# Performance work log

Measured on AMD Instinct MI355X. Metric: run time of the kernel, lower is better.

Reference implementation:

```python
import jax, jax.numpy as jnp
import numpy as np

N, E, D, H = 4096, 131072, 256, 8
DH = D // H  # head dim = 32


def layer_norm(x, g, b, eps=1e-5):
    mu = jnp.mean(x, axis=-1, keepdims=True)
    var = jnp.var(x, axis=-1, keepdims=True)
    return (x - mu) * jax.lax.rsqrt(var + eps) * g + b


def mlp2(x, w1, b1, w2, b2):
    # Linear -> GELU(exact) -> Linear (dropout is identity at inference)
    return jax.nn.gelu(x @ w1 + b1, approximate=False) @ w2 + b2


def setup_inputs() -> dict:
    key = jax.random.key(0)
    ks = iter(jax.random.split(key, 32))
    s = 0.02
    d = {
        'x': jax.random.normal(next(ks), (N, D), jnp.float32),
        'edge_index': jax.random.randint(next(ks), (2, E), 0, N, jnp.int32),
        'edge_attr': jax.random.normal(next(ks), (E, D), jnp.float32),
        # GINE eps
        'eps': jnp.zeros((1,), jnp.float32),
        # edge MLP (Linear weights stored [in, out])
        'e_w1': jax.random.normal(next(ks), (D, D), jnp.float32) * s,
        'e_b1': jnp.zeros((D,), jnp.float32),
        'e_w2': jax.random.normal(next(ks), (D, D), jnp.float32) * s,
        'e_b2': jnp.zeros((D,), jnp.float32),
        # update MLP
        'u_w1': jax.random.normal(next(ks), (D, D), jnp.float32) * s,
        'u_b1': jnp.zeros((D,), jnp.float32),
        'u_w2': jax.random.normal(next(ks), (D, D), jnp.float32) * s,
        'u_b2': jnp.zeros((D,), jnp.float32),
        # LayerNorms
        'ln_local_g': jnp.ones((D,), jnp.float32), 'ln_local_b': jnp.zeros((D,), jnp.float32),
        'ln_global_g': jnp.ones((D,), jnp.float32), 'ln_global_b': jnp.zeros((D,), jnp.float32),
        'ln_ffn_g': jnp.ones((D,), jnp.float32), 'ln_ffn_b': jnp.zeros((D,), jnp.float32),
        # MHA projections ([in, out])
        'wq': jax.random.normal(next(ks), (D, D), jnp.float32) * s,
        'wk': jax.random.normal(next(ks), (D, D), jnp.float32) * s,
        'wv': jax.random.normal(next(ks), (D, D), jnp.float32) * s,
        'bq': jnp.zeros((D,), jnp.float32), 'bk': jnp.zeros((D,), jnp.float32), 'bv': jnp.zeros((D,), jnp.float32),
        'wo': jax.random.normal(next(ks), (D, D), jnp.float32) * s,
        'bo': jnp.zeros((D,), jnp.float32),
        # FFN
        'f_w1': jax.random.normal(next(ks), (D, 4 * D), jnp.float32) * s,
        'f_b1': jnp.zeros((4 * D,), jnp.float32),
        'f_w2': jax.random.normal(next(ks), (4 * D, D), jnp.float32) * s,
        'f_b2': jnp.zeros((D,), jnp.float32),
    }
    return d


def reference(x, edge_index, edge_attr, eps,
              e_w1, e_b1, e_w2, e_b2, u_w1, u_b1, u_w2, u_b2,
              ln_local_g, ln_local_b, ln_global_g, ln_global_b, ln_ffn_g, ln_ffn_b,
              wq, wk, wv, bq, bk, bv, wo, bo,
              f_w1, f_b1, f_w2, f_b2):
    src, dst = edge_index[0], edge_index[1]
    n = x.shape[0]

    # ---- local GINE conv on pre-normed features ----
    h = layer_norm(x, ln_local_g, ln_local_b)
    messages = mlp2(h[src] + edge_attr, e_w1, e_b1, e_w2, e_b2)  # [E, D]
    aggregated = jax.ops.segment_sum(messages, dst, num_segments=n)  # [N, D]
    local = mlp2((1.0 + eps) * h + aggregated, u_w1, u_b1, u_w2, u_b2)
    x = x + local

    # ---- global multihead self-attention over all nodes ----
    g = layer_norm(x, ln_global_g, ln_global_b)
    q = (g @ wq + bq).reshape(n, H, DH)
    k = (g @ wk + bk).reshape(n, H, DH)
    v = (g @ wv + bv).reshape(n, H, DH)
    scores = jnp.einsum('nhd,mhd->hnm', q, k) / jnp.sqrt(jnp.float32(DH))
    attn = jax.nn.softmax(scores, axis=-1)
    ctx = jnp.einsum('hnm,mhd->nhd', attn, v).reshape(n, D)
    x = x + (ctx @ wo + bo)

    # ---- FFN ----
    x = x + mlp2(layer_norm(x, ln_ffn_g, ln_ffn_b), f_w1, f_b1, f_w2, f_b2)
    return x
```

## Files before the change

### kernel.cpp

```cpp
#include <hip/hip_runtime.h>
#include <math.h>

#define N_NODES 4096
#define N_EDGES 131072
#define XPAD    272

using bf16x8 = __attribute__((ext_vector_type(8))) __bf16;
using f32x4  = __attribute__((ext_vector_type(4))) float;
typedef unsigned short u16;

__device__ __forceinline__ u16 f2bf(float f) {
  union { __bf16 b; u16 u; } cv; cv.b = (__bf16)f; return cv.u;
}
__device__ __forceinline__ float bf2f(u16 h) {
  return __uint_as_float(((unsigned)h) << 16);
}
__device__ __forceinline__ float gelu_tanh(float x) {
  float t = x * x;
  float y = x * (1.5957691216057308f + 0.07135481627f * t);
  float e = __expf(y);
  return x - x / (1.0f + e);
}
__device__ __forceinline__ f32x4 mfma16(bf16x8 a, bf16x8 b, f32x4 c) {
  return __builtin_amdgcn_mfma_f32_16x16x32_bf16(a, b, c, 0, 0, 0);
}

struct WPtrs { const float* p[10]; };
struct OPtrs { float* o[4]; float* l; };

__global__ void setup_kernel(WPtrs w, u16* __restrict__ dst, float qscale,
                             const int* __restrict__ ei, int* __restrict__ deg,
                             const float* __restrict__ bq, const float* __restrict__ bk,
                             const float* __restrict__ bv, float* __restrict__ qkvbias) {
  int blk = blockIdx.x, t = threadIdx.x;
  if (blk < 512) {
    int tid = blk * 256 + t;
    int m, ci;
    if (tid < 32768)      { m = tid >> 13;                 ci = tid & 8191; }
    else if (tid < 57344) { m = 4 + ((tid - 32768) >> 13); ci = (tid - 32768) & 8191; }
    else if (tid < 65536) { m = 7; ci = tid - 57344; }
    else if (tid < 98304) { m = 8; ci = tid - 65536; }
    else                  { m = 9; ci = tid - 98304; }
    int Cols = (m == 8) ? 1024 : 256;
    int k8   = (m == 8) ? (ci >> 10) : (ci >> 8);
    int c    = (m == 8) ? (ci & 1023) : (ci & 255);
    const float* src = w.p[m] + (size_t)(k8 * 8) * Cols + c;
    float sc = (m == 4) ? qscale : 1.0f;
    u16 tmp[8];
#pragma unroll
    for (int j = 0; j < 8; ++j) tmp[j] = f2bf(src[(size_t)j * Cols] * sc);
    size_t off;
    if (m < 4)       off = (size_t)(m << 16) + (size_t)(k8 * 256 + c) * 8;
    else if (m < 7)  off = 262144 + (size_t)(k8 * 768 + (m - 4) * 256 + c) * 8;
    else if (m == 7) off = 458752 + (size_t)(k8 * 256 + c) * 8;
    else if (m == 8) off = 524288 + (size_t)(k8 * 1024 + c) * 8;
    else             off = 786432 + (size_t)(k8 * 256 + c) * 8;
    *(uint4*)(dst + off) = *(const uint4*)tmp;
  } else if (blk < 1024) {
    int e = (blk - 512) * 256 + t;
    atomicAdd(&deg[ei[N_EDGES + e]], 1);
  } else {
#pragma unroll
    for (int i = 0; i < 3; ++i) {
      int idx = i * 256 + t;
      qkvbias[idx] = idx < 256 ? bq[idx] * qscale : (idx < 512 ? bk[idx - 256] : bv[idx - 512]);
    }
  }
}

__global__ void scan_kernel(const int* __restrict__ deg, int* __restrict__ offs) {
  __shared__ int part[1024];
  int t = threadIdx.x;
  int base = t * 4;
  int a0 = deg[base], a1 = deg[base + 1], a2 = deg[base + 2], a3 = deg[base + 3];
  int s = a0 + a1 + a2 + a3;
  part[t] = s;
  __syncthreads();
  for (int off = 1; off < 1024; off <<= 1) {
    int v = (t >= off) ? part[t - off] : 0;
    __syncthreads();
    part[t] += v;
    __syncthreads();
  }
  int excl = part[t] - s;
  offs[base] = excl;
  offs[base + 1] = excl + a0;
  offs[base + 2] = excl + a0 + a1;
  offs[base + 3] = excl + a0 + a1 + a2;
  if (t == 1023) offs[4096] = part[1023];
}

__global__ void mid_kernel(const int* __restrict__ ei, const int* __restrict__ offs,
                           int* __restrict__ cnt, int* __restrict__ eperm,
                           int* __restrict__ dst_s, int* __restrict__ src_s,
                           const float* __restrict__ x, const float* __restrict__ g,
                           const float* __restrict__ b, float* __restrict__ hf,
                           u16* __restrict__ hb) {
  int blk = blockIdx.x, t = threadIdx.x;
  if (blk < 512) {
    int e = blk * 256 + t;
    int d = ei[N_EDGES + e];
    int p = offs[d] + atomicAdd(&cnt[d], 1);
    eperm[p] = e;
    dst_s[p] = d;
    src_s[p] = ei[e];
  } else {
    int row = blk - 512;
    float v = x[(size_t)row * 256 + t];
    float s1 = v, s2 = v * v;
#pragma unroll
    for (int o = 32; o > 0; o >>= 1) { s1 += __shfl_xor(s1, o); s2 += __shfl_xor(s2, o); }
    __shared__ float a1[4], a2[4];
    int wv = t >> 6, lane = t & 63;
    if (lane == 0) { a1[wv] = s1; a2[wv] = s2; }
    __syncthreads();
    s1 = a1[0] + a1[1] + a1[2] + a1[3];
    s2 = a2[0] + a2[1] + a2[2] + a2[3];
    float mean = s1 * (1.0f / 256.0f);
    float var  = s2 * (1.0f / 256.0f) - mean * mean;
    float rs = rsqrtf(var + 1e-5f);
    float o = (v - mean) * rs * g[t] + b[t];
    hf[(size_t)row * 256 + t] = o;
    hb[(size_t)row * 256 + t] = f2bf(o);
  }
}

__launch_bounds__(512, 4)
__global__ void edge_kernel(const u16* __restrict__ hb, const float* __restrict__ ea,
                            const int* __restrict__ eperm, const int* __restrict__ src_s,
                            const int* __restrict__ dst_s,
                            const u16* __restrict__ wp1, const float* __restrict__ b1,
                            const u16* __restrict__ wp2, const float* __restrict__ b2,
                            float* __restrict__ agg) {
  __shared__ __align__(16) u16 X[128 * XPAD];
  const f32x4 fzero = {0.f, 0.f, 0.f, 0.f};
  int t = threadIdx.x;
  int lane = t & 63, wv = t >> 6;
  int lr = lane & 15, lq = lane >> 4;
  int wr = wv >> 2, wc = wv & 3;
  int e0 = blockIdx.x * 128;
  int col0 = wc * 64;
  int row0 = wr * 64;

  const u16* b1ptr = wp1 + ((size_t)lq * 256 + col0 + lr) * 8;
  const u16* b2ptr = wp2 + ((size_t)lq * 256 + col0 + lr) * 8;
  bf16x8 bc[4], bn[4];
#pragma unroll
  for (int ct = 0; ct < 4; ++ct) bc[ct] = *(const bf16x8*)(b1ptr + ct * 128);

  int ci = (t & 31) * 8;
#pragma unroll
  for (int it = 0; it < 8; ++it) {
    int r = it * 16 + (t >> 5);
    int e = eperm[e0 + r];
    int s = src_s[e0 + r];
    const float* pa = ea + (size_t)e * 256 + ci;
    float4 a0 = *(const float4*)pa;
    float4 a1 = *(const float4*)(pa + 4);
    ushort4 h0 = *(const ushort4*)(hb + (size_t)s * 256 + ci);
    ushort4 h1 = *(const ushort4*)(hb + (size_t)s * 256 + ci + 4);
    u16 tmp[8];
    tmp[0] = f2bf(a0.x + bf2f(h0.x)); tmp[1] = f2bf(a0.y + bf2f(h0.y));
    tmp[2] = f2bf(a0.z + bf2f(h0.z)); tmp[3] = f2bf(a0.w + bf2f(h0.w));
    tmp[4] = f2bf(a1.x + bf2f(h1.x)); tmp[5] = f2bf(a1.y + bf2f(h1.y));
    tmp[6] = f2bf(a1.z + bf2f(h1.z)); tmp[7] = f2bf(a1.w + bf2f(h1.w));
    *(uint4*)&X[r * XPAD + ci] = *(const uint4*)tmp;
  }
  __syncthreads();

  f32x4 acc[4][4];
#pragma unroll
  for (int i = 0; i < 4; ++i)
#pragma unroll
    for (int j = 0; j < 4; ++j) acc[i][j] = fzero;

#pragma unroll
  for (int ks = 0; ks < 8; ++ks) {
    if (ks < 7) {
#pragma unroll
      for (int ct = 0; ct < 4; ++ct)
        bn[ct] = *(const bf16x8*)(b1ptr + (size_t)(ks + 1) * 8192 + ct * 128);
    }
    bf16x8 a[4];
#pragma unroll
    for (int rt = 0; rt < 4; ++rt)
      a[rt] = *(const bf16x8*)&X[(row0 + rt * 16 + lr) * XPAD + ks * 32 + lq * 8];
#pragma unroll
    for (int ct = 0; ct < 4; ++ct)
#pragma unroll
      for (int rt = 0; rt < 4; ++rt) acc[rt][ct] = mfma16(a[rt], bc[ct], acc[rt][ct]);
#pragma unroll
    for (int ct = 0; ct < 4; ++ct) bc[ct] = bn[ct];
  }
#pragma unroll
  for (int ct = 0; ct < 4; ++ct) bn[ct] = *(const bf16x8*)(b2ptr + ct * 128);
  __syncthreads();

#pragma unroll
  for (int ct = 0; ct < 4; ++ct) {
    int c = col0 + ct * 16 + lr;
    float bb = b1[c];
#pragma unroll
    for (int rt = 0; rt < 4; ++rt)
#pragma unroll
      for (int r = 0; r < 4; ++r) {
        int row = row0 + rt * 16 + lq * 4 + r;
        X[row * XPAD + c] = f2bf(gelu_tanh(acc[rt][ct][r] + bb));
      }
  }
#pragma unroll
  for (int ct = 0; ct < 4; ++ct) bc[ct] = bn[ct];
  __syncthreads();

#pragma unroll
  for (int i = 0; i < 4; ++i)
#pragma unroll
    for (int j = 0; j < 4; ++j) acc[i][j] = fzero;
#pragma unroll
  for (int ks = 0; ks < 8; ++ks) {
    if (ks < 7) {
#pragma unroll
      for (int ct = 0; ct < 4; ++ct)
        bn[ct] = *(const bf16x8*)(b2ptr + (size_t)(ks + 1) * 8192 + ct * 128);
    }
    bf16x8 a[4];
#pragma unroll
    for (int rt = 0; rt < 4; ++rt)
      a[rt] = *(const bf16x8*)&X[(row0 + rt * 16 + lr) * XPAD + ks * 32 + lq * 8];
#pragma unroll
    for (int ct = 0; ct < 4; ++ct)
#pragma unroll
      for (int rt = 0; rt < 4; ++rt) acc[rt][ct] = mfma16(a[rt], bc[ct], acc[rt][ct]);
#pragma unroll
    for (int ct = 0; ct < 4; ++ct) bc[ct] = bn[ct];
  }
  __syncthreads();

#pragma unroll
  for (int ct = 0; ct < 4; ++ct) {
    int c = col0 + ct * 16 + lr;
    float bb = b2[c];
#pragma unroll
    for (int rt = 0; rt < 4; ++rt)
#pragma unroll
      for (int r = 0; r < 4; ++r) {
        int row = row0 + rt * 16 + lq * 4 + r;
        X[row * XPAD + c] = f2bf(acc[rt][ct][r] + bb);
      }
  }
  __syncthreads();

  {
    int c4 = (t & 63) * 4;
    int rbeg = wv * 16;
    float run0 = 0.f, run1 = 0.f, run2 = 0.f, run3 = 0.f;
    int cur = dst_s[e0 + rbeg];
    for (int r = rbeg; r < rbeg + 16; ++r) {
      int d = dst_s[e0 + r];
      if (d != cur) {
        float* p = &agg[(size_t)cur * 256 + c4];
        atomicAdd(p + 0, run0); atomicAdd(p + 1, run1);
        atomicAdd(p + 2, run2); atomicAdd(p + 3, run3);
        run0 = run1 = run2 = run3 = 0.f;
        cur = d;
      }
      ushort4 xv = *(const ushort4*)&X[r * XPAD + c4];
      run0 += bf2f(xv.x); run1 += bf2f(xv.y); run2 += bf2f(xv.z); run3 += bf2f(xv.w);
    }
    float* p = &agg[(size_t)cur * 256 + c4];
    atomicAdd(p + 0, run0); atomicAdd(p + 1, run1);
    atomicAdd(p + 2, run2); atomicAdd(p + 3, run3);
  }
}

__launch_bounds__(256, 2)
__global__ void update_kernel(const float* __restrict__ hf, const float* __restrict__ agg,
                              const float* __restrict__ epsp, const float* __restrict__ xin,
                              const u16* __restrict__ wp1, const float* __restrict__ b1,
                              const u16* __restrict__ wp2, const float* __restrict__ b2,
                              const float* __restrict__ lng, const float* __restrict__ lnb,
                              float* __restrict__ x1, u16* __restrict__ gb) {
  __shared__ __align__(16) u16 X[64 * XPAD];
  __shared__ float S1[64][4], S2[64][4], MUs[64], RSs[64];
  const f32x4 fzero = {0.f, 0.f, 0.f, 0.f};
  int t = threadIdx.x;
  int lane = t & 63, wv = t >> 6;
  int lr = lane & 15, lq = lane >> 4;
  int n0 = blockIdx.x * 64;
  int col0 = wv * 64;
  float epv = 1.0f + epsp[0];
  const u16* b1ptr = wp1 + ((size_t)lq * 256 + col0 + lr) * 8;
  const u16* b2ptr = wp2 + ((size_t)lq * 256 + col0 + lr) * 8;
  bf16x8 bc[4], bn[4];
#pragma unroll
  for (int ct = 0; ct < 4; ++ct) bc[ct] = *(const bf16x8*)(b1ptr + ct * 128);
  {
    int c4 = (t & 63) * 4;
#pragma unroll
    for (int ii = 0; ii < 16; ++ii) {
      int r = ii * 4 + wv;
      float4 h = *(const float4*)(hf + (size_t)(n0 + r) * 256 + c4);
      float4 a = *(const float4*)(agg + (size_t)(n0 + r) * 256 + c4);
      *(ushort4*)&X[r * XPAD + c4] =
          make_ushort4(f2bf(epv * h.x + a.x), f2bf(epv * h.y + a.y),
                       f2bf(epv * h.z + a.z), f2bf(epv * h.w + a.w));
    }
  }
  __syncthreads();
  f32x4 acc[4][4];
#pragma unroll
  for (int i = 0; i < 4; ++i)
#pragma unroll
    for (int j = 0; j < 4; ++j) acc[i][j] = fzero;
#pragma unroll
  for (int ks = 0; ks < 8; ++ks) {
    if (ks < 7) {
#pragma unroll
      for (int ct = 0; ct < 4; ++ct)
        bn[ct] = *(const bf16x8*)(b1ptr + (size_t)(ks + 1) * 8192 + ct * 128);
    }
    bf16x8 a[4];
#pragma unroll
    for (int rt = 0; rt < 4; ++rt)
      a[rt] = *(const bf16x8*)&X[(rt * 16 + lr) * XPAD + ks * 32 + lq * 8];
#pragma unroll
    for (int ct = 0; ct < 4; ++ct)
#pragma unroll
      for (int rt = 0; rt < 4; ++rt) acc[rt][ct] = mfma16(a[rt], bc[ct], acc[rt][ct]);
#pragma unroll
    for (int ct = 0; ct < 4; ++ct) bc[ct] = bn[ct];
  }
#pragma unroll
  for (int ct = 0; ct < 4; ++ct) bn[ct] = *(const bf16x8*)(b2ptr + ct * 128);
  __syncthreads();
#pragma unroll
  for (int ct = 0; ct < 4; ++ct) {
    int c = col0 + ct * 16 + lr;
    float bb = b1[c];
#pragma unroll
    for (int rt = 0; rt < 4; ++rt)
#pragma unroll
      for (int r = 0; r < 4; ++r) {
        int row = rt * 16 + lq * 4 + r;
        X[row * XPAD + c] = f2bf(gelu_tanh(acc[rt][ct][r] + bb));
      }
  }
#pragma unroll
  for (int ct = 0; ct < 4; ++ct) bc[ct] = bn[ct];
  __syncthreads();
#pragma unroll
  for (int i = 0; i < 4; ++i)
#pragma unroll
    for (int j = 0; j < 4; ++j) acc[i][j] = fzero;
#pragma unroll
  for (int ks = 0; ks < 8; ++ks) {
    if (ks < 7) {
#pragma unroll
      for (int ct = 0; ct < 4; ++ct)
        bn[ct] = *(const bf16x8*)(b2ptr + (size_t)(ks + 1) * 8192 + ct * 128);
    }
    bf16x8 a[4];
#pragma unroll
    for (int rt = 0; rt < 4; ++rt)
      a[rt] = *(const bf16x8*)&X[(rt * 16 + lr) * XPAD + ks * 32 + lq * 8];
#pragma unroll
    for (int ct = 0; ct < 4; ++ct)
#pragma unroll
      for (int rt = 0; rt < 4; ++rt) acc[rt][ct] = mfma16(a[rt], bc[ct], acc[rt][ct]);
#pragma unroll
    for (int ct = 0; ct < 4; ++ct) bc[ct] = bn[ct];
  }
  float bb2[4];
#pragma unroll
  for (int ct = 0; ct < 4; ++ct) bb2[ct] = b2[col0 + ct * 16 + lr];
#pragma unroll
  for (int rt = 0; rt < 4; ++rt)
#pragma unroll
    for (int r = 0; r < 4; ++r) {
      int row = rt * 16 + lq * 4 + r;
      int grow = n0 + row;
      float p1 = 0.f, p2 = 0.f;
#pragma unroll
      for (int ct = 0; ct < 4; ++ct) {
        int c = col0 + ct * 16 + lr;
        float v = acc[rt][ct][r] + bb2[ct] + xin[(size_t)grow * 256 + c];
        x1[(size_t)grow * 256 + c] = v;
        acc[rt][ct][r] = v;
        p1 += v; p2 += v * v;
      }
#pragma unroll
      for (int o = 1; o < 16; o <<= 1) { p1 += __shfl_xor(p1, o); p2 += __shfl_xor(p2, o); }
      if (lr == 0) { S1[row][wv] = p1; S2[row][wv] = p2; }
    }
  __syncthreads();
  if (t < 64) {
    float s1 = S1[t][0] + S1[t][1] + S1[t][2] + S1[t][3];
    float s2 = S2[t][0] + S2[t][1] + S2[t][2] + S2[t][3];
    float mu = s1 * (1.0f / 256.0f);
    float var = s2 * (1.0f / 256.0f) - mu * mu;
    MUs[t] = mu;
    RSs[t] = rsqrtf(var + 1e-5f);
  }
  __syncthreads();
  float gv[4], bv[4];
#pragma unroll
  for (int ct = 0; ct < 4; ++ct) {
    int c = col0 + ct * 16 + lr;
    gv[ct] = lng[c]; bv[ct] = lnb[c];
  }
#pragma unroll
  for (int rt = 0; rt < 4; ++rt)
#pragma unroll
    for (int r = 0; r < 4; ++r) {
      int row = rt * 16 + lq * 4 + r;
      int grow = n0 + row;
      float mu = MUs[row], rs = RSs[row];
#pragma unroll
      for (int ct = 0; ct < 4; ++ct) {
        int c = col0 + ct * 16 + lr;
        gb[(size_t)grow * 256 + c] = f2bf((acc[rt][ct][r] - mu) * rs * gv[ct] + bv[ct]);
      }
    }
}

template <int ROWS, bool GELU_F, bool RES, bool OUTB, bool LNF, bool QKV>
__launch_bounds__(256, 2)
__global__ void gemm_kernel(const u16* __restrict__ A, int lda,
                            const u16* __restrict__ Wp, int K, int WCols,
                            const float* __restrict__ bias, float scale,
                            const float* __restrict__ res,
                            const float* __restrict__ lng, const float* __restrict__ lnb,
                            float* __restrict__ outf, u16* __restrict__ outh,
                            u16* __restrict__ outh2, u16* __restrict__ vtp, int ldo) {
  __shared__ __align__(16) u16 X[ROWS * XPAD];
  __shared__ float S1[LNF ? ROWS : 1][4], S2[LNF ? ROWS : 1][4];
  __shared__ float MUs[LNF ? ROWS : 1], RSs[LNF ? ROWS : 1];
  constexpr int RT = ROWS / 16;
  const f32x4 fzero = {0.f, 0.f, 0.f, 0.f};
  int t = threadIdx.x;
  int lane = t & 63, wv = t >> 6;
  int lr = lane & 15, lq = lane >> 4;
  int r0 = blockIdx.x * ROWS;
  int cb = blockIdx.y * 256;
  f32x4 acc[RT][4];
#pragma unroll
  for (int i = 0; i < RT; ++i)
#pragma unroll
    for (int j = 0; j < 4; ++j) acc[i][j] = fzero;
  const u16* bptr = Wp + ((size_t)lq * WCols + cb + wv * 64 + lr) * 8;
  bf16x8 bc[4], bn[4];
#pragma unroll
  for (int ct = 0; ct < 4; ++ct) bc[ct] = *(const bf16x8*)(bptr + ct * 128);
  int rr = t >> 5, c8 = (t & 31) * 8;
  for (int kc = 0; kc < K; kc += 256) {
#pragma unroll
    for (int ii = 0; ii < ROWS / 8; ++ii) {
      int r = ii * 8 + rr;
      *(uint4*)&X[r * XPAD + c8] = *(const uint4*)(A + (size_t)(r0 + r) * lda + kc + c8);
    }
    __syncthreads();
#pragma unroll
    for (int ks = 0; ks < 8; ++ks) {
      bool more = (ks < 7) || (kc + 256 < K);
      if (more) {
        size_t koff = (ks < 7) ? ((size_t)(kc >> 3) + (ks + 1) * 4) * WCols
                               : ((size_t)((kc + 256) >> 3)) * WCols;
#pragma unroll
        for (int ct = 0; ct < 4; ++ct)
          bn[ct] = *(const bf16x8*)(bptr + (koff + ct * 16) * 8);
      }
      bf16x8 a[RT];
#pragma unroll
      for (int rt = 0; rt < RT; ++rt)
        a[rt] = *(const bf16x8*)&X[(rt * 16 + lr) * XPAD + ks * 32 + lq * 8];
#pragma unroll
      for (int ct = 0; ct < 4; ++ct)
#pragma unroll
        for (int rt = 0; rt < RT; ++rt) acc[rt][ct] = mfma16(a[rt], bc[ct], acc[rt][ct]);
#pragma unroll
      for (int ct = 0; ct < 4; ++ct) bc[ct] = bn[ct];
    }
    __syncthreads();
  }
  if (QKV) {
    int y = blockIdx.y;
#pragma unroll
    for (int ct = 0; ct < 4; ++ct) {
      int c = cb + wv * 64 + ct * 16 + lr;
      float bb = bias[c];
#pragma unroll
      for (int rt = 0; rt < RT; ++rt)
#pragma unroll
        for (int r = 0; r < 4; ++r) {
          int row = r0 + rt * 16 + lq * 4 + r;
          u16 hv = f2bf(acc[rt][ct][r] + bb);
          if (y == 0)      outh[(size_t)row * 256 + c] = hv;
          else if (y == 1) outh2[(size_t)row * 256 + (c - 256)] = hv;
          else             vtp[(size_t)(c - 512) * 4096 + row] = hv;
        }
    }
  } else if (!LNF) {
#pragma unroll
    for (int ct = 0; ct < 4; ++ct) {
      int c = cb + wv * 64 + ct * 16 + lr;
      float bb = bias[c];
#pragma unroll
      for (int rt = 0; rt < RT; ++rt)
#pragma unroll
        for (int r = 0; r < 4; ++r) {
          int row = r0 + rt * 16 + lq * 4 + r;
          float v = (acc[rt][ct][r] + bb) * scale;
          if (GELU_F) v = gelu_tanh(v);
          if (RES) v += res[(size_t)row * 256 + c];
          if (OUTB) outh[(size_t)row * ldo + c] = f2bf(v);
          else      outf[(size_t)row * ldo + c] = v;
        }
    }
  } else {
    float bb[4];
#pragma unroll
    for (int ct = 0; ct < 4; ++ct) bb[ct] = bias[wv * 64 + ct * 16 + lr];
#pragma unroll
    for (int rt = 0; rt < RT; ++rt)
#pragma unroll
      for (int r = 0; r < 4; ++r) {
        int row = rt * 16 + lq * 4 + r;
        int grow = r0 + row;
        float p1 = 0.f, p2 = 0.f;
#pragma unroll
        for (int ct = 0; ct < 4; ++ct) {
          int c = wv * 64 + ct * 16 + lr;
          float v = acc[rt][ct][r] + bb[ct];
          if (RES) v += res[(size_t)grow * 256 + c];
          outf[(size_t)grow * 256 + c] = v;
          acc[rt][ct][r] = v;
          p1 += v; p2 += v * v;
        }
#pragma unroll
        for (int o = 1; o < 16; o <<= 1) { p1 += __shfl_xor(p1, o); p2 += __shfl_xor(p2, o); }
        if (lr == 0) { S1[row][wv] = p1; S2[row][wv] = p2; }
      }
    __syncthreads();
    if (t < ROWS) {
      float s1 = S1[t][0] + S1[t][1] + S1[t][2] + S1[t][3];
      float s2 = S2[t][0] + S2[t][1] + S2[t][2] + S2[t][3];
      float mu = s1 * (1.0f / 256.0f);
      float var = s2 * (1.0f / 256.0f) - mu * mu;
      MUs[t] = mu;
      RSs[t] = rsqrtf(var + 1e-5f);
    }
    __syncthreads();
    float gv[4], bv[4];
#pragma unroll
    for (int ct = 0; ct < 4; ++ct) {
      int c = wv * 64 + ct * 16 + lr;
      gv[ct] = lng[c]; bv[ct] = lnb[c];
    }
#pragma unroll
    for (int rt = 0; rt < RT; ++rt)
#pragma unroll
      for (int r = 0; r < 4; ++r) {
        int row = rt * 16 + lq * 4 + r;
        int grow = r0 + row;
        float mu = MUs[row], rs = RSs[row];
#pragma unroll
        for (int ct = 0; ct < 4; ++ct) {
          int c = wv * 64 + ct * 16 + lr;
          outh[(size_t)grow * ldo + c] = f2bf((acc[rt][ct][r] - mu) * rs * gv[ct] + bv[ct]);
        }
      }
  }
}

__launch_bounds__(256, 6)
__global__ void attn_kernel(const u16* __restrict__ qb, const u16* __restrict__ kb,
                            const u16* __restrict__ vT, OPtrs op) {
  __shared__ u16 Kt[64 * 40];
  __shared__ u16 Vt[32 * 72];
  __shared__ float P32[4][1024];
  const f32x4 fzero = {0.f, 0.f, 0.f, 0.f};
  int t = threadIdx.x;
  int lane = t & 63, wv = t >> 6;
  int lr = lane & 15, lq = lane >> 4;
  int head = blockIdx.y;
  int z = blockIdx.z;
  int q0 = blockIdx.x * 64 + wv * 16;
  int kbase = z * 1024;
  bf16x8 qf = *(const bf16x8*)(qb + (size_t)(q0 + lr) * 256 + head * 32 + lq * 8);
  f32x4 o0 = fzero, o1 = fzero;
  float l_i[4] = {0.f, 0.f, 0.f, 0.f};
  int kkey = t >> 2, kdp = (t & 3) * 8;
  int vd = t >> 3, vkc = (t & 7) * 8;
  const u16* vbase = vT + (size_t)(head * 32 + vd) * 4096;
  int psw = (lr >> 2) & 3;
  float* pw = &P32[wv][0];
  uint4 kreg = *(const uint4*)(kb + (size_t)(kbase + kkey) * 256 + head * 32 + kdp);
  uint4 vreg = *(const uint4*)(vbase + kbase + vkc);
  for (int it = 0; it < 16; ++it) {
    __syncthreads();
    *(uint4*)&Kt[kkey * 40 + kdp] = kreg;
    *(uint4*)&Vt[vd * 72 + vkc]   = vreg;
    if (it < 15) {
      int kn = kbase + (it + 1) * 64;
      kreg = *(const uint4*)(kb + (size_t)(kn + kkey) * 256 + head * 32 + kdp);
      vreg = *(const uint4*)(vbase + kn + vkc);
    }
    __syncthreads();
    f32x4 s[4];
#pragma unroll
    for (int ct = 0; ct < 4; ++ct) {
      bf16x8 bk = *(const bf16x8*)&Kt[(ct * 16 + lr) * 40 + lq * 8];
      s[ct] = mfma16(qf, bk, fzero);
    }
#pragma unroll
    for (int ct = 0; ct < 4; ++ct)
#pragma unroll
      for (int r = 0; r < 4; ++r) s[ct][r] = __expf(s[ct][r]);
#pragma unroll
    for (int r = 0; r < 4; ++r) {
      float ps = (s[0][r] + s[1][r]) + (s[2][r] + s[3][r]);
#pragma unroll
      for (int d = 1; d < 16; d <<= 1) ps += __shfl_xor(ps, d);
      l_i[r] += ps;
    }
#pragma unroll
    for (int ct = 0; ct < 4; ++ct) {
      int col = ct * 16 + lr;
      int w = (((col >> 2) ^ lq) << 2) + (col & 3);
#pragma unroll
      for (int r = 0; r < 4; ++r) pw[(lq * 4 + r) * 64 + w] = s[ct][r];
    }
#pragma unroll
    for (int kp = 0; kp < 2; ++kp) {
      int cch = kp * 8 + lq * 2;
      f32x4 f0 = *(const f32x4*)&pw[lr * 64 + ((cch ^ psw) << 2)];
      f32x4 f1 = *(const f32x4*)&pw[lr * 64 + (((cch + 1) ^ psw) << 2)];
      bf16x8 pa;
#pragma unroll
      for (int j = 0; j < 4; ++j) { pa[j] = (__bf16)f0[j]; pa[j + 4] = (__bf16)f1[j]; }
      bf16x8 v0 = *(const bf16x8*)&Vt[lr * 72 + kp * 32 + lq * 8];
      bf16x8 v1 = *(const bf16x8*)&Vt[(16 + lr) * 72 + kp * 32 + lq * 8];
      o0 = mfma16(pa, v0, o0);
      o1 = mfma16(pa, v1, o1);
    }
  }
  float* ob = op.o[z];
  float* lp = op.l + z * 32768;
#pragma unroll
  for (int r = 0; r < 4; ++r) {
    int row = q0 + lq * 4 + r;
    ob[(size_t)row * 256 + head * 32 + lr]      = o0[r];
    ob[(size_t)row * 256 + head * 32 + 16 + lr] = o1[r];
    if (lr == 0) lp[row * 8 + head] = l_i[r];
  }
}

__global__ void attn_merge(OPtrs op, u16* __restrict__ ctx) {
  int c = threadIdx.x;
  int head = c >> 5;
#pragma unroll
  for (int r = 0; r < 4; ++r) {
    int row = blockIdx.x * 4 + r;
    size_t idx = (size_t)row * 256 + c;
    float o = op.o[0][idx] + op.o[1][idx] + op.o[2][idx] + op.o[3][idx];
    int li = row * 8 + head;
    float l = op.l[li] + op.l[32768 + li] + op.l[65536 + li] + op.l[98304 + li];
    ctx[idx] = f2bf(o / l);
  }
}

extern "C" void kernel_launch(void* const* d_in, const int* in_sizes, int n_in,
                              void* d_out, int out_size, void* d_ws, size_t ws_size,
                              hipStream_t stream) {
  const float* x         = (const float*)d_in[0];
  const int*   ei        = (const int*)d_in[1];
  const float* edge_attr = (const float*)d_in[2];
  const float* eps       = (const float*)d_in[3];
  const float* e_w1 = (const float*)d_in[4];
  const float* e_b1 = (const float*)d_in[5];
  const float* e_w2 = (const float*)d_in[6];
  const float* e_b2 = (const float*)d_in[7];
  const float* u_w1 = (const float*)d_in[8];
  const float* u_b1 = (const float*)d_in[9];
  const float* u_w2 = (const float*)d_in[10];
  const float* u_b2 = (const float*)d_in[11];
  const float* ln_local_g  = (const float*)d_in[12];
  const float* ln_local_b  = (const float*)d_in[13];
  const float* ln_global_g = (const float*)d_in[14];
  const float* ln_global_b = (const float*)d_in[15];
  const float* ln_ffn_g    = (const float*)d_in[16];
  const float* ln_ffn_b    = (const float*)d_in[17];
  const float* wq = (const float*)d_in[18];
  const float* wk = (const float*)d_in[19];
  const float* wv = (const float*)d_in[20];
  const float* bq = (const float*)d_in[21];
  const float* bk = (const float*)d_in[22];
  const float* bv = (const float*)d_in[23];
  const float* wo = (const float*)d_in[24];
  const float* bo = (const float*)d_in[25];
  const float* f_w1 = (const float*)d_in[26];
  const float* f_b1 = (const float*)d_in[27];
  const float* f_w2 = (const float*)d_in[28];
  const float* f_b2 = (const float*)d_in[29];

  char* ws = (char*)d_ws;
  u16*   WP      = (u16*)(ws + 0);
  float* agg     = (float*)(ws + (2u  << 20));
  int*   deg     = (int*)(ws + (6u  << 20));
  int*   cnt     = (int*)(ws + (6u  << 20) + (16u << 10));
  int*   offs    = (int*)(ws + (6u  << 20) + (32u << 10));
  float* qkvbias = (float*)(ws + (6u << 20) + (64u << 10));
  float* hf      = (float*)(ws + (7u  << 20));
  float* x1      = (float*)(ws + (11u << 20));
  u16*   gb      = (u16*)(ws + (15u << 20));
  u16*   qbuf    = (u16*)(ws + (17u << 20));
  u16*   kbuf    = (u16*)(ws + (19u << 20));
  u16*   vTb     = (u16*)(ws + (21u << 20));
  u16*   ctxb    = (u16*)(ws + (23u << 20));
  float* x2      = (float*)(ws + (25u << 20));
  u16*   yb      = (u16*)(ws + (29u << 20));
  u16*   hid     = (u16*)(ws + (31u << 20));
  int*   eperm   = (int*)(ws + (39u << 20));
  int*   dst_s   = (int*)(ws + (39u << 20) + (512u << 10));
  int*   src_s   = (int*)(ws + (40u << 20));
  u16*   hb      = (u16*)(ws + (40u << 20) + (512u << 10));

  const size_t O_EW1 = 0, O_EW2 = 65536, O_UW1 = 131072, O_UW2 = 196608,
               O_QKV = 262144, O_WO = 458752, O_FW1 = 524288, O_FW2 = 786432;
  const float qscale = 0.17677669529663687f;

  hipMemsetAsync(agg, 0, (4u << 20) + (32u << 10), stream);

  WPtrs wp;
  wp.p[0] = e_w1; wp.p[1] = e_w2; wp.p[2] = u_w1; wp.p[3] = u_w2;
  wp.p[4] = wq;   wp.p[5] = wk;   wp.p[6] = wv;   wp.p[7] = wo;
  wp.p[8] = f_w1; wp.p[9] = f_w2;
  setup_kernel<<<1025, 256, 0, stream>>>(wp, WP, qscale, ei, deg, bq, bk, bv, qkvbias);
  scan_kernel<<<1, 1024, 0, stream>>>(deg, offs);
  mid_kernel<<<4608, 256, 0, stream>>>(ei, offs, cnt, eperm, dst_s, src_s,
                                       x, ln_local_g, ln_local_b, hf, hb);

  edge_kernel<<<N_EDGES / 128, 512, 0, stream>>>(hb, edge_attr, eperm, src_s, dst_s,
                                                 WP + O_EW1, e_b1, WP + O_EW2, e_b2, agg);

  update_kernel<<<N_NODES / 64, 256, 0, stream>>>(hf, agg, eps, x,
                                                  WP + O_UW1, u_b1, WP + O_UW2, u_b2,
                                                  ln_global_g, ln_global_b, x1, gb);

  gemm_kernel<64, false, false, true, false, true><<<dim3(64, 3), 256, 0, stream>>>(
      gb, 256, WP + O_QKV, 256, 768, qkvbias, 1.0f, nullptr, nullptr, nullptr,
      nullptr, qbuf, kbuf, vTb, 256);

  OPtrs op;
  op.o[0] = agg;
  op.o[1] = hf;
  op.o[2] = x2;
  op.o[3] = (float*)(ws + (31u << 20));
  op.l    = (float*)(ws + (29u << 20));
  attn_kernel<<<dim3(64, 8, 4), 256, 0, stream>>>(qbuf, kbuf, vTb, op);
  attn_merge<<<N_NODES / 4, 256, 0, stream>>>(op, ctxb);

  gemm_kernel<32, false, true, false, true, false><<<dim3(128, 1), 256, 0, stream>>>(
      ctxb, 256, WP + O_WO, 256, 256, bo, 1.0f, x1, ln_ffn_g, ln_ffn_b, x2, yb,
      nullptr, nullptr, 256);

  gemm_kernel<64, true, false, true, false, false><<<dim3(64, 4), 256, 0, stream>>>(
      yb, 256, WP + O_FW1, 256, 1024, f_b1, 1.0f, nullptr, nullptr, nullptr,
      nullptr, hid, nullptr, nullptr, 1024);

  gemm_kernel<32, false, true, false, false, false><<<dim3(128, 1), 256, 0, stream>>>(
      hid, 1024, WP + O_FW2, 1024, 256, f_b2, 1.0f, x2, nullptr, nullptr,
      (float*)d_out, nullptr, nullptr, nullptr, 256);
}
```

Before: 527.4 us.

## Segment-group edge aggregation with direct stores for fully owned destination nodes

The per-block segment reduction in the edge kernel now finds destination-group boundaries with a wave ballot and assigns whole groups to waves. It no longer has each wave scan a fixed 16-row slice. When a block holds every edge of a destination node, the sum is written with a plain float4 store instead of four atomics. This cuts atomic traffic and splits groups across fewer atomic targets. It adds shared-memory bookkeeping, an extra sync-dependent setup and lookups into the offsets array.

```diff
diff --git a/kernel.cpp b/kernel.cpp
--- a/kernel.cpp
+++ b/kernel.cpp
@@ -128,11 +128,14 @@
 __launch_bounds__(512, 4)
 __global__ void edge_kernel(const u16* __restrict__ hb, const float* __restrict__ ea,
                             const int* __restrict__ eperm, const int* __restrict__ src_s,
-                            const int* __restrict__ dst_s,
+                            const int* __restrict__ dst_s, const int* __restrict__ offs,
                             const u16* __restrict__ wp1, const float* __restrict__ b1,
                             const u16* __restrict__ wp2, const float* __restrict__ b2,
                             float* __restrict__ agg) {
   __shared__ __align__(16) u16 X[128 * XPAD];
+  __shared__ int gstart[130];
+  __shared__ unsigned long long bm[2];
+  __shared__ int Gs;
   const f32x4 fzero = {0.f, 0.f, 0.f, 0.f};
   int t = threadIdx.x;
   int lane = t & 63, wv = t >> 6;
@@ -166,6 +169,14 @@
     tmp[6] = f2bf(a1.z + bf2f(h1.z)); tmp[7] = f2bf(a1.w + bf2f(h1.w));
     *(uint4*)&X[r * XPAD + ci] = *(const uint4*)tmp;
   }
+  int flag = 0;
+  if (t < 128) {
+    int d  = dst_s[e0 + t];
+    int dp = (t == 0) ? -1 : dst_s[e0 + t - 1];
+    flag = (d != dp) ? 1 : 0;
+  }
+  unsigned long long m = __ballot(flag);
+  if (wv < 2 && lane == 0) bm[wv] = m;
   __syncthreads();
 
   f32x4 acc[4][4];
@@ -194,6 +205,16 @@
   }
 #pragma unroll
   for (int ct = 0; ct < 4; ++ct) bn[ct] = *(const bf16x8*)(b2ptr + ct * 128);
+  if (t < 128 && flag) {
+    int idx = __popcll(bm[wv] & ((1ull << lane) - 1));
+    if (wv == 1) idx += __popcll(bm[0]);
+    gstart[idx] = t;
+  }
+  if (t == 0) {
+    int g = __popcll(bm[0]) + __popcll(bm[1]);
+    Gs = g;
+    gstart[g] = 128;
+  }
   __syncthreads();
 
 #pragma unroll
@@ -251,25 +272,25 @@
   __syncthreads();
 
   {
-    int c4 = (t & 63) * 4;
-    int rbeg = wv * 16;
-    float run0 = 0.f, run1 = 0.f, run2 = 0.f, run3 = 0.f;
-    int cur = dst_s[e0 + rbeg];
-    for (int r = rbeg; r < rbeg + 16; ++r) {
-      int d = dst_s[e0 + r];
-      if (d != cur) {
-        float* p = &agg[(size_t)cur * 256 + c4];
+    int G = Gs;
+    int c4 = lane * 4;
+    for (int gi = wv; gi < G; gi += 8) {
+      int rs = gstart[gi], re = gstart[gi + 1];
+      int d = dst_s[e0 + rs];
+      float run0 = 0.f, run1 = 0.f, run2 = 0.f, run3 = 0.f;
+      for (int r = rs; r < re; ++r) {
+        ushort4 xv = *(const ushort4*)&X[r * XPAD + c4];
+        run0 += bf2f(xv.x); run1 += bf2f(xv.y); run2 += bf2f(xv.z); run3 += bf2f(xv.w);
+      }
+      bool full = (offs[d] == e0 + rs) && (offs[d + 1] == e0 + re);
+      float* p = &agg[(size_t)d * 256 + c4];
+      if (full) {
+        *(float4*)p = make_float4(run0, run1, run2, run3);
+      } else {
         atomicAdd(p + 0, run0); atomicAdd(p + 1, run1);
         atomicAdd(p + 2, run2); atomicAdd(p + 3, run3);
-        run0 = run1 = run2 = run3 = 0.f;
-        cur = d;
-      }
-      ushort4 xv = *(const ushort4*)&X[r * XPAD + c4];
-      run0 += bf2f(xv.x); run1 += bf2f(xv.y); run2 += bf2f(xv.z); run3 += bf2f(xv.w);
-    }
-    float* p = &agg[(size_t)cur * 256 + c4];
-    atomicAdd(p + 0, run0); atomicAdd(p + 1, run1);
-    atomicAdd(p + 2, run2); atomicAdd(p + 3, run3);
+      }
+    }
   }
 }
 
@@ -740,7 +761,7 @@
   mid_kernel<<<4608, 256, 0, stream>>>(ei, offs, cnt, eperm, dst_s, src_s,
                                        x, ln_local_g, ln_local_b, hf, hb);
 
-  edge_kernel<<<N_EDGES / 128, 512, 0, stream>>>(hb, edge_attr, eperm, src_s, dst_s,
+  edge_kernel<<<N_EDGES / 128, 512, 0, stream>>>(hb, edge_attr, eperm, src_s, dst_s, offs,
                                                  WP + O_EW1, e_b1, WP + O_EW2, e_b2, agg);
 
   update_kernel<<<N_NODES / 64, 256, 0, stream>>>(hf, agg, eps, x,
```

Measured after the change: 510.9 us. 1.03x faster.
